# Performance work log

Measured on AMD Instinct MI355X. Metric: run time of the kernel, lower is better.

## Reference

```python
import jax, jax.numpy as jnp
import numpy as np

N, IN, HID, OUT, E, G = 20000, 256, 256, 128, 320000, 64


def setup_inputs() -> dict:
    key = jax.random.key(0)
    ks = jax.random.split(key, 16)
    s = 0.05
    x = jax.random.normal(ks[0], (N, IN), jnp.float32)
    edge_index = jax.random.randint(ks[1], (2, E), 0, N, dtype=jnp.int32)
    batch = jnp.sort(jax.random.randint(ks[2], (N,), 0, G, dtype=jnp.int32))
    return {
        "x": x,
        "edge_index": edge_index,
        "batch": batch,
        "num_graphs": G,
        "W1": jax.random.normal(ks[3], (HID, IN), jnp.float32) * s,
        "b1": jnp.zeros((HID,), jnp.float32),
        "W2": jax.random.normal(ks[4], (HID, HID), jnp.float32) * s,
        "b2": jnp.zeros((HID,), jnp.float32),
        "W3": jax.random.normal(ks[5], (HID, HID), jnp.float32) * s,
        "b3": jnp.zeros((HID,), jnp.float32),
        "W4": jax.random.normal(ks[6], (OUT, HID), jnp.float32) * s,
        "b4": jnp.zeros((OUT,), jnp.float32),
        "lin_w": jax.random.normal(ks[7], (1, OUT), jnp.float32) * s,
        "lin_b": jnp.zeros((1,), jnp.float32),
    }


def reference(x, edge_index, batch, num_graphs, W1, b1, W2, b2, W3, b3, W4, b4, lin_w, lin_b):
    row, col = edge_index[0], edge_index[1]
    n = x.shape[0]
    # degree-based symmetric-ish norm (as in source: degree of row only)
    deg = jax.ops.segment_sum(jnp.ones((row.shape[0],), x.dtype), row, num_segments=n)
    deg_inv_sqrt = deg ** -0.5  # 0-degree -> inf, matching torch deg.pow(-0.5)
    norm = (deg_inv_sqrt[row] * deg_inv_sqrt[col])[:, None]  # [E,1]

    def gcn_layer(h, W, b):
        h = h @ W.T + b                                  # dense linear [N,out]
        msgs = norm * h[row]                             # gather + scale [E,out]
        return jax.ops.segment_sum(msgs, col, num_segments=n)  # scatter-add

    h = gcn_layer(x, W1, b1)
    h = gcn_layer(h, W2, b2)
    h = gcn_layer(h, W3, b3)
    h = gcn_layer(h, W4, b4)

    # to_dense_batch(...).mean(dim=1): sum per graph / max graph size (padded mean)
    sums = jax.ops.segment_sum(h, batch, num_segments=num_graphs)          # [G,OUT]
    counts = jax.ops.segment_sum(jnp.ones((n,), h.dtype), batch, num_segments=num_graphs)
    x_new = sums / jnp.max(counts)
    return x_new @ lin_w.T + lin_b  # [G,1]
```

## Files before the change

kernel.cpp:

```cpp
#include <hip/hip_runtime.h>
#include <math.h>

#define NN      20000
#define IN_DIM  256
#define HID_DIM 256
#define OUT_DIM 128
#define EE      320000
#define GG      64

#define P_H     16
#define CHUNK   (EE / P_H)
#define NW      10000
#define PSTRIDE 10240
#define HISTB   (2 * P_H)
#define CHB     16
#define MGB     40
#define MVB     1250
#define SCB2    313
#define GB      313


__device__ __forceinline__ int ldi_mall(const int* p) {
  return __hip_atomic_load(p, __ATOMIC_RELAXED, __HIP_MEMORY_SCOPE_AGENT);
}

__global__ __launch_bounds__(1024) void k_hist_chain(
    const int* __restrict__ erow, const int* __restrict__ ecol,
    unsigned int* __restrict__ pdeg, unsigned int* __restrict__ pccnt,
    unsigned short* __restrict__ rankb, int* __restrict__ zctr,
    const float* __restrict__ W1, const float* __restrict__ b1,
    const float* __restrict__ W2, const float* __restrict__ b2,
    const float* __restrict__ W3, const float* __restrict__ b3,
    const float* __restrict__ W4, const float* __restrict__ b4,
    const float* __restrict__ lw, float* __restrict__ q1g,
    float* __restrict__ dv) {
  __shared__ __align__(16) char smem[40960];
  const int bid = blockIdx.x, tid = threadIdx.x;

  if (bid < HISTB) {
    if (bid == 0 && tid < 320) zctr[tid] = 0;
    unsigned int* h = (unsigned int*)smem;
    const int  p   = bid & (P_H - 1);
    const bool isc = bid >= P_H;
    const int* src = isc ? ecol : erow;
    unsigned int* slab = (isc ? pccnt : pdeg) + (size_t)p * PSTRIDE;
    for (int w = tid; w < NW; w += 1024) h[w] = 0u;
    __syncthreads();
    const int base = p * CHUNK;
    for (int i = tid; i < CHUNK; i += 1024) {
      int v = src[base + i];
      int sh = (v & 1) << 4;
      unsigned int old = atomicAdd(&h[v >> 1], 1u << sh);
      if (isc) rankb[base + i] = (unsigned short)((old >> sh) & 0xFFFFu);
    }
    __syncthreads();
    for (int w = tid; w < NW; w += 1024) slab[w] = h[w];
    return;
  }

  const int cb = bid - HISTB;
  float* fs  = (float*)smem;
  float* lws = fs;
  float* qa  = fs + 128;
  float* qb  = fs + 384;
  float* qc  = fs + 640;
  float* qd  = fs + 896;
  float* part = fs + 1152;
  float* red  = fs + 2176;
  const int j = tid & 255, tq = tid >> 8;

  if (tid < 128) lws[tid] = lw[tid];
  __syncthreads();

  auto gemv = [&](const float* W, const float* qin, float* qout, int K) {
    const int quarter = K >> 2, t0 = tq * quarter;
    float s = 0.f;
#pragma unroll 4
    for (int m = 0; m < quarter; ++m) {
      int t = t0 + m;
      s += W[(size_t)t * 256 + j] * qin[t];
    }
    part[tq * 256 + j] = s;
    __syncthreads();
    if (tq == 0) qout[j] = part[j] + part[256 + j] + part[512 + j] + part[768 + j];
    __syncthreads();
  };

  gemv(W4, lws, qa, OUT_DIM);
  gemv(W3, qa, qb, HID_DIM);
  gemv(W2, qb, qc, HID_DIM);
  gemv(W1, qc, qd, HID_DIM);
  if (tid < 16) q1g[cb * 16 + tid] = qd[cb * 16 + tid];

  if (cb == 0) {
    auto dot = [&](const float* a, const float* bl, int K, float* dst) {
      float p = (tid < K) ? a[tid] * bl[tid] : 0.f;
#pragma unroll
      for (int off = 32; off; off >>= 1) p += __shfl_down(p, off);
      if ((tid & 63) == 0) red[tid >> 6] = p;
      __syncthreads();
      if (tid == 0) { float s = 0.f; for (int k = 0; k < 16; ++k) s += red[k]; *dst = s; }
      __syncthreads();
    };
    dot(b1, qc, HID_DIM, &dv[0]);
    dot(b2, qb, HID_DIM, &dv[1]);
    dot(b3, qa, HID_DIM, &dv[2]);
    dot(b4, lws, OUT_DIM, &dv[3]);
  }
}

__global__ __launch_bounds__(1024) void k_mssc_mv(
    const unsigned int* __restrict__ pdeg, const unsigned int* __restrict__ pccnt,
    int* __restrict__ deg, int* __restrict__ ccnt,
    unsigned short* __restrict__ chunkoff, int* __restrict__ mergedone,
    int* __restrict__ scandone, int* __restrict__ cstart,
    const int* __restrict__ batch, float* __restrict__ outcnt,
    const float* __restrict__ x, const float* __restrict__ q1,
    float* __restrict__ u0,
    const int* __restrict__ erow, const int* __restrict__ ecol,
    const unsigned short* __restrict__ rankb, int2* __restrict__ sedge) {
  int bid = blockIdx.x, tid = threadIdx.x, lane = tid & 63, wid = tid >> 6;

  if (bid == 0) {
    if (tid == 0) {
      while (__hip_atomic_load(mergedone, __ATOMIC_RELAXED, __HIP_MEMORY_SCOPE_AGENT) < MGB)
        __builtin_amdgcn_s_sleep(1);
      (void)__hip_atomic_load(mergedone, __ATOMIC_ACQUIRE, __HIP_MEMORY_SCOPE_AGENT);
    }
    __syncthreads();
    __shared__ int ws[16];
    const int PER = 20;
    int base = tid * PER;
    int v[PER]; int sum = 0;
#pragma unroll
    for (int i = 0; i < PER; ++i) {
      int idx = base + i;
      v[i] = (idx < NN) ? ldi_mall(&ccnt[idx]) : 0;
      sum += v[i];
    }
    int incl = sum;
#pragma unroll
    for (int off = 1; off < 64; off <<= 1) { int t = __shfl_up(incl, off); if (lane >= off) incl += t; }
    if (lane == 63) ws[wid] = incl;
    __syncthreads();
    if (tid == 0) { int r = 0; for (int k = 0; k < 16; ++k) { int t = ws[k]; ws[k] = r; r += t; } }
    __syncthreads();
    int run = ws[wid] + incl - sum;
#pragma unroll
    for (int i = 0; i < PER; ++i) {
      int idx = base + i;
      if (idx < NN) cstart[idx] = run;
      run += v[i];
    }
    if (tid == 1023) cstart[NN] = run;
    __syncthreads();
    if (tid == 0)
      __hip_atomic_fetch_add(scandone, 1, __ATOMIC_RELEASE, __HIP_MEMORY_SCOPE_AGENT);
    return;
  }

  if (bid <= MGB) {
    int w0 = (bid - 1) * 250;
    for (int w = w0 + tid; w < w0 + 250; w += 1024) {
      unsigned int dlo = 0, dhi = 0, clo = 0, chi = 0;
      const int c0 = 2 * w, c1 = 2 * w + 1;
#pragma unroll
      for (int p = 0; p < P_H; ++p) {
        unsigned int ud = pdeg[(size_t)p * PSTRIDE + w];
        unsigned int uc = pccnt[(size_t)p * PSTRIDE + w];
        dlo += ud & 0xFFFFu; dhi += ud >> 16;
        chunkoff[(size_t)c0 * P_H + p] = (unsigned short)clo;
        chunkoff[(size_t)c1 * P_H + p] = (unsigned short)chi;
        clo += uc & 0xFFFFu; chi += uc >> 16;
      }
      deg[c0]  = (int)dlo; deg[c1]  = (int)dhi;
      ccnt[c0] = (int)clo; ccnt[c1] = (int)chi;
    }
    __syncthreads();
    if (tid == 0)
      __hip_atomic_fetch_add(mergedone, 1, __ATOMIC_RELEASE, __HIP_MEMORY_SCOPE_AGENT);
    return;
  }

  if (bid == MGB + 1) {
    for (int base = 0; base < NN; base += 1024) {
      int n = base + tid;
      int b = -1; float cn = 0.f;
      if (n < NN) { b = batch[n]; cn = 1.f; }
#pragma unroll
      for (int off = 1; off < 64; off <<= 1) {
        float c2 = __shfl_up(cn, off);
        int   b2 = __shfl_up(b, off);
        if (lane >= off && b2 == b) cn += c2;
      }
      int bn = __shfl_down(b, 1);
      if (((lane == 63) || (bn != b)) && b >= 0) atomicAdd(&outcnt[b], cn);
    }
    return;
  }

  if (bid < MGB + 2 + MVB) {
    int r = (bid - (MGB + 2)) * 16 + wid;
    if (r >= NN) return;
    const float4 xv = *(const float4*)(x + (size_t)r * IN_DIM + lane * 4);
    const float4 qv = *(const float4*)(q1 + lane * 4);
    float s = xv.x * qv.x + xv.y * qv.y + xv.z * qv.z + xv.w * qv.w;
#pragma unroll
    for (int off = 32; off; off >>= 1) s += __shfl_down(s, off);
    if (lane == 0) u0[r] = s;
    return;
  }

  if (tid == 0) {
    while (__hip_atomic_load(scandone, __ATOMIC_RELAXED, __HIP_MEMORY_SCOPE_AGENT) < 1)
      __builtin_amdgcn_s_sleep(1);
    (void)__hip_atomic_load(scandone, __ATOMIC_ACQUIRE, __HIP_MEMORY_SCOPE_AGENT);
  }
  __syncthreads();
  int e = (bid - (MGB + 2 + MVB)) * 1024 + tid;
  if (e >= EE) return;
  int r = erow[e], c = ecol[e];
  int p = e / CHUNK;
  int slot = cstart[c] + (int)chunkoff[(size_t)c * P_H + p] + (int)rankb[e];
  float dr = (float)deg[r], dc = (float)deg[c];
  float val = (1.0f / sqrtf(dr)) * (1.0f / sqrtf(dc));
  sedge[slot] = make_int2(r, __float_as_int(val));
}

__global__ __launch_bounds__(256) void k_gather(
    const int* __restrict__ cstart, const int2* __restrict__ sedge,
    const float* __restrict__ uin, const float* __restrict__ dptr,
    float* __restrict__ uout) {
  int gid = blockIdx.x * 256 + threadIdx.x;
  int n = gid >> 2, l = gid & 3;
  if (n >= NN) return;
  int s0 = cstart[n], s1 = cstart[n + 1];
  float acc = 0.f, es = 0.f;
  int s = s0 + l;
  if (s < s1) {
    int2 ev = sedge[s];
    float uv = uin[ev.x];
    for (s += 4; s < s1; s += 4) {
      int2 evn = sedge[s];
      float un = uin[evn.x];
      float v = __int_as_float(ev.y);
      acc += v * uv;
      es  += v;
      ev = evn; uv = un;
    }
    float v = __int_as_float(ev.y);
    acc += v * uv;
    es  += v;
  }
  acc += __shfl_xor(acc, 1); es += __shfl_xor(es, 1);
  acc += __shfl_xor(acc, 2); es += __shfl_xor(es, 2);
  if (l == 0) uout[n] = acc + dptr[0] * es;
}

__global__ __launch_bounds__(256) void k_gather_pool(
    const int* __restrict__ cstart, const int2* __restrict__ sedge,
    const float* __restrict__ uin, const float* __restrict__ dptr,
    const int* __restrict__ batch, float* __restrict__ outsum) {
  int gid = blockIdx.x * 256 + threadIdx.x;
  int lane = threadIdx.x & 63;
  int n = gid >> 2, l = gid & 3;
  float pv = 0.f; int b = -1;
  if (n < NN) {
    int s0 = cstart[n], s1 = cstart[n + 1];
    float acc = 0.f, es = 0.f;
    int s = s0 + l;
    if (s < s1) {
      int2 ev = sedge[s];
      float uv = uin[ev.x];
      for (s += 4; s < s1; s += 4) {
        int2 evn = sedge[s];
        float un = uin[evn.x];
        float v = __int_as_float(ev.y);
        acc += v * uv;
        es  += v;
        ev = evn; uv = un;
      }
      float v = __int_as_float(ev.y);
      acc += v * uv;
      es  += v;
    }
    acc += __shfl_xor(acc, 1); es += __shfl_xor(es, 1);
    acc += __shfl_xor(acc, 2); es += __shfl_xor(es, 2);
    b = batch[n];
    if (l == 0) pv = acc + dptr[0] * es;
  }
#pragma unroll
  for (int off = 1; off < 64; off <<= 1) {
    float s2 = __shfl_up(pv, off);
    int   b2 = __shfl_up(b, off);
    if (lane >= off && b2 == b) pv += s2;
  }
  int bn = __shfl_down(b, 1);
  if (((lane == 63) || (bn != b)) && b >= 0) atomicAdd(&outsum[b], pv);
}

__global__ __launch_bounds__(64) void k_finalize(
    const float* __restrict__ outsum, const float* __restrict__ outcnt,
    const float* __restrict__ lb, float* __restrict__ out) {
  int g = threadIdx.x;
  float m = outcnt[g];
#pragma unroll
  for (int off = 32; off; off >>= 1) m = fmaxf(m, __shfl_xor(m, off));
  out[g] = outsum[g] / m + lb[0];
}

extern "C" void kernel_launch(void* const* d_in, const int* in_sizes, int n_in,
                              void* d_out, int out_size, void* d_ws, size_t ws_size,
                              hipStream_t stream) {
  (void)in_sizes; (void)n_in; (void)out_size; (void)ws_size;
  const float* x     = (const float*)d_in[0];
  const int*   erow  = (const int*)d_in[1];
  const int*   ecol  = ((const int*)d_in[1]) + EE;
  const int*   batch = (const int*)d_in[2];
  const float* W1 = (const float*)d_in[4];
  const float* b1 = (const float*)d_in[5];
  const float* W2 = (const float*)d_in[6];
  const float* b2 = (const float*)d_in[7];
  const float* W3 = (const float*)d_in[8];
  const float* b3 = (const float*)d_in[9];
  const float* W4 = (const float*)d_in[10];
  const float* b4 = (const float*)d_in[11];
  const float* lw = (const float*)d_in[12];
  const float* lb = (const float*)d_in[13];
  float* out = (float*)d_out;

  const size_t PN = 80128;
  char* w = (char*)d_ws;
  float* outsum    = (float*)w;  w += 256;
  float* outcnt    = (float*)w;  w += 256;
  int*   done      = (int*)w;    w += 256;
  int*   mergedone = (int*)w;    w += 256;
  int*   scandone  = (int*)w;    w += 256;
  (void)done;
  int*   deg    = (int*)w;    w += PN;
  int*   ccnt   = (int*)w;    w += PN;
  int*   cstart = (int*)w;    w += PN + 256;
  int2*  sedge  = (int2*)w;   w += (size_t)EE * 8;
  unsigned int*   pdeg  = (unsigned int*)w;   w += (size_t)P_H * PSTRIDE * 4;
  unsigned int*   pccnt = (unsigned int*)w;   w += (size_t)P_H * PSTRIDE * 4;
  unsigned short* chunkoff = (unsigned short*)w; w += (size_t)NN * P_H * 2;
  unsigned short* rankb    = (unsigned short*)w; w += (size_t)EE * 2;
  float* q1 = (float*)w;  w += 1024;
  float* dv = (float*)w;  w += 256;
  float* u0 = (float*)w;  w += PN;
  float* u1 = (float*)w;  w += PN;
  float* u2 = (float*)w;  w += PN;
  float* u3 = (float*)w;  w += PN;

  k_hist_chain<<<HISTB + CHB, 1024, 0, stream>>>(erow, ecol, pdeg, pccnt,
                                                 rankb, (int*)d_ws,
                                                 W1, b1, W2, b2, W3, b3, W4, b4,
                                                 lw, q1, dv);
  k_mssc_mv<<<MGB + 2 + MVB + SCB2, 1024, 0, stream>>>(
      pdeg, pccnt, deg, ccnt, chunkoff, mergedone, scandone, cstart,
      batch, outcnt, x, q1, u0, erow, ecol, rankb, sedge);
  k_gather<<<GB, 256, 0, stream>>>(cstart, sedge, u0, dv + 0, u1);
  k_gather<<<GB, 256, 0, stream>>>(cstart, sedge, u1, dv + 1, u2);
  k_gather<<<GB, 256, 0, stream>>>(cstart, sedge, u2, dv + 2, u3);
  k_gather_pool<<<GB, 256, 0, stream>>>(cstart, sedge, u3, dv + 3, batch, outsum);
  k_finalize<<<1, 64, 0, stream>>>(outsum, outcnt, lb, out);
}
```

Baseline: 85.30 us.

## Move histogram merge and prefix scan into front kernel using inter-block flags

The per-partition histogram merge and the exclusive scan of column counts move from the second kernel into the first. They wait on histdone/mergedone counters there, so they overlap with the weight-chain GEMV blocks. The scatter blocks in the second kernel no longer spin on a scan flag, because the kernel boundary now orders them. Counters are zeroed with a hipMemsetAsync instead of inside the kernel, which adds a memset launch and relies on all hist blocks being co-resident with the spinning merge blocks.

```diff
diff --git a/kernel.cpp b/kernel.cpp
--- a/kernel.cpp
+++ b/kernel.cpp
@@ -13,8 +13,8 @@
 #define NW      10000
 #define PSTRIDE 10240
 #define HISTB   (2 * P_H)
+#define MGB     40
 #define CHB     16
-#define MGB     40
 #define MVB     1250
 #define SCB2    313
 #define GB      313
@@ -23,11 +23,17 @@
 __device__ __forceinline__ int ldi_mall(const int* p) {
   return __hip_atomic_load(p, __ATOMIC_RELAXED, __HIP_MEMORY_SCOPE_AGENT);
 }
-
-__global__ __launch_bounds__(1024) void k_hist_chain(
+__device__ __forceinline__ unsigned int ldu_mall(const unsigned int* p) {
+  return __hip_atomic_load(p, __ATOMIC_RELAXED, __HIP_MEMORY_SCOPE_AGENT);
+}
+
+__global__ __launch_bounds__(1024) void k_front(
     const int* __restrict__ erow, const int* __restrict__ ecol,
     unsigned int* __restrict__ pdeg, unsigned int* __restrict__ pccnt,
-    unsigned short* __restrict__ rankb, int* __restrict__ zctr,
+    unsigned short* __restrict__ rankb,
+    int* __restrict__ histdone, int* __restrict__ mergedone,
+    int* __restrict__ deg, int* __restrict__ ccnt,
+    unsigned short* __restrict__ chunkoff, int* __restrict__ cstart,
     const float* __restrict__ W1, const float* __restrict__ b1,
     const float* __restrict__ W2, const float* __restrict__ b2,
     const float* __restrict__ W3, const float* __restrict__ b3,
@@ -36,9 +42,9 @@
     float* __restrict__ dv) {
   __shared__ __align__(16) char smem[40960];
   const int bid = blockIdx.x, tid = threadIdx.x;
+  const int lane = tid & 63, wid = tid >> 6;
 
   if (bid < HISTB) {
-    if (bid == 0 && tid < 320) zctr[tid] = 0;
     unsigned int* h = (unsigned int*)smem;
     const int  p   = bid & (P_H - 1);
     const bool isc = bid >= P_H;
@@ -55,10 +61,77 @@
     }
     __syncthreads();
     for (int w = tid; w < NW; w += 1024) slab[w] = h[w];
-    return;
-  }
-
-  const int cb = bid - HISTB;
+    __syncthreads();
+    if (tid == 0)
+      __hip_atomic_fetch_add(histdone, 1, __ATOMIC_RELEASE, __HIP_MEMORY_SCOPE_AGENT);
+    return;
+  }
+
+  if (bid < HISTB + MGB) {
+    if (tid == 0) {
+      while (__hip_atomic_load(histdone, __ATOMIC_RELAXED, __HIP_MEMORY_SCOPE_AGENT) < HISTB)
+        __builtin_amdgcn_s_sleep(1);
+      (void)__hip_atomic_load(histdone, __ATOMIC_ACQUIRE, __HIP_MEMORY_SCOPE_AGENT);
+    }
+    __syncthreads();
+    int w0 = (bid - HISTB) * 250;
+    for (int w = w0 + tid; w < w0 + 250; w += 1024) {
+      unsigned int dlo = 0, dhi = 0, clo = 0, chi = 0;
+      const int c0 = 2 * w, c1 = 2 * w + 1;
+#pragma unroll
+      for (int p = 0; p < P_H; ++p) {
+        unsigned int ud = ldu_mall(&pdeg[(size_t)p * PSTRIDE + w]);
+        unsigned int uc = ldu_mall(&pccnt[(size_t)p * PSTRIDE + w]);
+        dlo += ud & 0xFFFFu; dhi += ud >> 16;
+        chunkoff[(size_t)c0 * P_H + p] = (unsigned short)clo;
+        chunkoff[(size_t)c1 * P_H + p] = (unsigned short)chi;
+        clo += uc & 0xFFFFu; chi += uc >> 16;
+      }
+      deg[c0]  = (int)dlo; deg[c1]  = (int)dhi;
+      ccnt[c0] = (int)clo; ccnt[c1] = (int)chi;
+    }
+    __syncthreads();
+    if (tid == 0)
+      __hip_atomic_fetch_add(mergedone, 1, __ATOMIC_RELEASE, __HIP_MEMORY_SCOPE_AGENT);
+    return;
+  }
+
+  if (bid == HISTB + MGB) {
+    if (tid == 0) {
+      while (__hip_atomic_load(mergedone, __ATOMIC_RELAXED, __HIP_MEMORY_SCOPE_AGENT) < MGB)
+        __builtin_amdgcn_s_sleep(1);
+      (void)__hip_atomic_load(mergedone, __ATOMIC_ACQUIRE, __HIP_MEMORY_SCOPE_AGENT);
+    }
+    __syncthreads();
+    __shared__ int ws[16];
+    const int PER = 20;
+    int base = tid * PER;
+    int v[PER]; int sum = 0;
+#pragma unroll
+    for (int i = 0; i < PER; ++i) {
+      int idx = base + i;
+      v[i] = (idx < NN) ? ldi_mall(&ccnt[idx]) : 0;
+      sum += v[i];
+    }
+    int incl = sum;
+#pragma unroll
+    for (int off = 1; off < 64; off <<= 1) { int t = __shfl_up(incl, off); if (lane >= off) incl += t; }
+    if (lane == 63) ws[wid] = incl;
+    __syncthreads();
+    if (tid == 0) { int r = 0; for (int k = 0; k < 16; ++k) { int t = ws[k]; ws[k] = r; r += t; } }
+    __syncthreads();
+    int run = ws[wid] + incl - sum;
+#pragma unroll
+    for (int i = 0; i < PER; ++i) {
+      int idx = base + i;
+      if (idx < NN) cstart[idx] = run;
+      run += v[i];
+    }
+    if (tid == 1023) cstart[NN] = run;
+    return;
+  }
+
+  const int cb = bid - (HISTB + MGB + 1);
   float* fs  = (float*)smem;
   float* lws = fs;
   float* qa  = fs + 128;
@@ -109,80 +182,17 @@
   }
 }
 
-__global__ __launch_bounds__(1024) void k_mssc_mv(
-    const unsigned int* __restrict__ pdeg, const unsigned int* __restrict__ pccnt,
-    int* __restrict__ deg, int* __restrict__ ccnt,
-    unsigned short* __restrict__ chunkoff, int* __restrict__ mergedone,
-    int* __restrict__ scandone, int* __restrict__ cstart,
+__global__ __launch_bounds__(1024) void k_cnt_mv_scatter(
     const int* __restrict__ batch, float* __restrict__ outcnt,
     const float* __restrict__ x, const float* __restrict__ q1,
     float* __restrict__ u0,
     const int* __restrict__ erow, const int* __restrict__ ecol,
+    const int* __restrict__ deg, const int* __restrict__ cstart,
+    const unsigned short* __restrict__ chunkoff,
     const unsigned short* __restrict__ rankb, int2* __restrict__ sedge) {
   int bid = blockIdx.x, tid = threadIdx.x, lane = tid & 63, wid = tid >> 6;
 
   if (bid == 0) {
-    if (tid == 0) {
-      while (__hip_atomic_load(mergedone, __ATOMIC_RELAXED, __HIP_MEMORY_SCOPE_AGENT) < MGB)
-        __builtin_amdgcn_s_sleep(1);
-      (void)__hip_atomic_load(mergedone, __ATOMIC_ACQUIRE, __HIP_MEMORY_SCOPE_AGENT);
-    }
-    __syncthreads();
-    __shared__ int ws[16];
-    const int PER = 20;
-    int base = tid * PER;
-    int v[PER]; int sum = 0;
-#pragma unroll
-    for (int i = 0; i < PER; ++i) {
-      int idx = base + i;
-      v[i] = (idx < NN) ? ldi_mall(&ccnt[idx]) : 0;
-      sum += v[i];
-    }
-    int incl = sum;
-#pragma unroll
-    for (int off = 1; off < 64; off <<= 1) { int t = __shfl_up(incl, off); if (lane >= off) incl += t; }
-    if (lane == 63) ws[wid] = incl;
-    __syncthreads();
-    if (tid == 0) { int r = 0; for (int k = 0; k < 16; ++k) { int t = ws[k]; ws[k] = r; r += t; } }
-    __syncthreads();
-    int run = ws[wid] + incl - sum;
-#pragma unroll
-    for (int i = 0; i < PER; ++i) {
-      int idx = base + i;
-      if (idx < NN) cstart[idx] = run;
-      run += v[i];
-    }
-    if (tid == 1023) cstart[NN] = run;
-    __syncthreads();
-    if (tid == 0)
-      __hip_atomic_fetch_add(scandone, 1, __ATOMIC_RELEASE, __HIP_MEMORY_SCOPE_AGENT);
-    return;
-  }
-
-  if (bid <= MGB) {
-    int w0 = (bid - 1) * 250;
-    for (int w = w0 + tid; w < w0 + 250; w += 1024) {
-      unsigned int dlo = 0, dhi = 0, clo = 0, chi = 0;
-      const int c0 = 2 * w, c1 = 2 * w + 1;
-#pragma unroll
-      for (int p = 0; p < P_H; ++p) {
-        unsigned int ud = pdeg[(size_t)p * PSTRIDE + w];
-        unsigned int uc = pccnt[(size_t)p * PSTRIDE + w];
-        dlo += ud & 0xFFFFu; dhi += ud >> 16;
-        chunkoff[(size_t)c0 * P_H + p] = (unsigned short)clo;
-        chunkoff[(size_t)c1 * P_H + p] = (unsigned short)chi;
-        clo += uc & 0xFFFFu; chi += uc >> 16;
-      }
-      deg[c0]  = (int)dlo; deg[c1]  = (int)dhi;
-      ccnt[c0] = (int)clo; ccnt[c1] = (int)chi;
-    }
-    __syncthreads();
-    if (tid == 0)
-      __hip_atomic_fetch_add(mergedone, 1, __ATOMIC_RELEASE, __HIP_MEMORY_SCOPE_AGENT);
-    return;
-  }
-
-  if (bid == MGB + 1) {
     for (int base = 0; base < NN; base += 1024) {
       int n = base + tid;
       int b = -1; float cn = 0.f;
@@ -199,8 +209,8 @@
     return;
   }
 
-  if (bid < MGB + 2 + MVB) {
-    int r = (bid - (MGB + 2)) * 16 + wid;
+  if (bid < 1 + MVB) {
+    int r = (bid - 1) * 16 + wid;
     if (r >= NN) return;
     const float4 xv = *(const float4*)(x + (size_t)r * IN_DIM + lane * 4);
     const float4 qv = *(const float4*)(q1 + lane * 4);
@@ -211,13 +221,7 @@
     return;
   }
 
-  if (tid == 0) {
-    while (__hip_atomic_load(scandone, __ATOMIC_RELAXED, __HIP_MEMORY_SCOPE_AGENT) < 1)
-      __builtin_amdgcn_s_sleep(1);
-    (void)__hip_atomic_load(scandone, __ATOMIC_ACQUIRE, __HIP_MEMORY_SCOPE_AGENT);
-  }
-  __syncthreads();
-  int e = (bid - (MGB + 2 + MVB)) * 1024 + tid;
+  int e = (bid - (1 + MVB)) * 1024 + tid;
   if (e >= EE) return;
   int r = erow[e], c = ecol[e];
   int p = e / CHUNK;
@@ -333,10 +337,11 @@
   char* w = (char*)d_ws;
   float* outsum    = (float*)w;  w += 256;
   float* outcnt    = (float*)w;  w += 256;
-  int*   done      = (int*)w;    w += 256;
+  int*   histdone  = (int*)w;    w += 256;
   int*   mergedone = (int*)w;    w += 256;
-  int*   scandone  = (int*)w;    w += 256;
-  (void)done;
+  int*   spare     = (int*)w;    w += 256;
+  (void)spare;
+  size_t zbytes = (size_t)(w - (char*)d_ws);
   int*   deg    = (int*)w;    w += PN;
   int*   ccnt   = (int*)w;    w += PN;
   int*   cstart = (int*)w;    w += PN + 256;
@@ -352,13 +357,13 @@
   float* u2 = (float*)w;  w += PN;
   float* u3 = (float*)w;  w += PN;
 
-  k_hist_chain<<<HISTB + CHB, 1024, 0, stream>>>(erow, ecol, pdeg, pccnt,
-                                                 rankb, (int*)d_ws,
-                                                 W1, b1, W2, b2, W3, b3, W4, b4,
-                                                 lw, q1, dv);
-  k_mssc_mv<<<MGB + 2 + MVB + SCB2, 1024, 0, stream>>>(
-      pdeg, pccnt, deg, ccnt, chunkoff, mergedone, scandone, cstart,
-      batch, outcnt, x, q1, u0, erow, ecol, rankb, sedge);
+  hipMemsetAsync(d_ws, 0, zbytes, stream);
+  k_front<<<HISTB + MGB + 1 + CHB, 1024, 0, stream>>>(
+      erow, ecol, pdeg, pccnt, rankb, histdone, mergedone,
+      deg, ccnt, chunkoff, cstart,
+      W1, b1, W2, b2, W3, b3, W4, b4, lw, q1, dv);
+  k_cnt_mv_scatter<<<1 + MVB + SCB2, 1024, 0, stream>>>(
+      batch, outcnt, x, q1, u0, erow, ecol, deg, cstart, chunkoff, rankb, sedge);
   k_gather<<<GB, 256, 0, stream>>>(cstart, sedge, u0, dv + 0, u1);
   k_gather<<<GB, 256, 0, stream>>>(cstart, sedge, u1, dv + 1, u2);
   k_gather<<<GB, 256, 0, stream>>>(cstart, sedge, u2, dv + 2, u3);
```

Result: slower. 90.61 us (+6.2%).
